# Optimization experiments

Hardware: AMD Instinct MI355X
Metric: run time of the kernel (lower is better)

Reference implementation:

```python
import jax, jax.numpy as jnp
import numpy as np

IN_CH, OUT_CH, MODES1, MODES2 = 64, 64, 32, 32
B, H, W = 16, 256, 256


def setup_inputs() -> dict:
    key = jax.random.key(0)
    k = jax.random.split(key, 5)
    scale = (1.0 / (2 * IN_CH)) ** 0.5
    wshape = (IN_CH, OUT_CH, MODES1, MODES2)
    return {
        "x": jax.random.normal(k[0], (B, IN_CH, H, W), dtype=jnp.float32),
        "weights_pos_re": scale * jax.random.normal(k[1], wshape, dtype=jnp.float32),
        "weights_pos_im": scale * jax.random.normal(k[2], wshape, dtype=jnp.float32),
        "weights_neg_re": scale * jax.random.normal(k[3], wshape, dtype=jnp.float32),
        "weights_neg_im": scale * jax.random.normal(k[4], wshape, dtype=jnp.float32),
        "out_h": H,
        "out_w": W,
    }


def reference(x, weights_pos_re, weights_pos_im, weights_neg_re, weights_neg_im, out_h, out_w):
    b, c_in, in_h, in_w = x.shape
    wp = weights_pos_re + 1j * weights_pos_im  # complex64 [i, o, m1, m2]
    wn = weights_neg_re + 1j * weights_neg_im
    # rfft2 with norm='forward' divides by n (matches torch.fft.rfft2 norm='forward')
    x_ft = jnp.fft.rfft2(x, norm="forward")  # [b, i, in_h, in_w//2+1] complex64
    m1 = min(MODES1, in_h // 2, out_h // 2)
    m2 = min(MODES2, x_ft.shape[-1], out_w // 2 + 1)
    # truncated-mode complex channel mixing on low-frequency corners
    top = jnp.einsum("bixy,ioxy->boxy", x_ft[:, :, :m1, :m2], wp[:, :, :m1, :m2])
    bot = jnp.einsum("bixy,ioxy->boxy", x_ft[:, :, -m1:, :m2], wn[:, :, :m1, :m2])
    out_ft = jnp.zeros((b, OUT_CH, out_h, out_w // 2 + 1), dtype=jnp.complex64)
    out_ft = out_ft.at[:, :, :m1, :m2].set(top)
    out_ft = out_ft.at[:, :, -m1:, :m2].set(bot)
    # irfft2 with norm='forward' multiplies by n
    return jnp.fft.irfft2(out_ft, s=(out_h, out_w), norm="forward")
```

## Files before the change

kernel.cpp:

```cpp
#include <hip/hip_runtime.h>
#include <math.h>

#define PI_F 3.14159265358979323846f


static constexpr int T_FA  = 0;
static constexpr int T_FE  = 16384;
static constexpr int T_FBC = 32768;
static constexpr int T_FBS = 49152;
static constexpr int T_FD1 = 65536;
static constexpr int T_FD2 = 98304;
static constexpr int T_X2  = 131072;
static constexpr int T_CC  = 131072 + 4194304;

typedef __attribute__((ext_vector_type(8))) __bf16 bf16x8;
typedef __attribute__((ext_vector_type(4))) float f32x4;

union B4 { __bf16 b[4]; uint2 u; };

__global__ __launch_bounds__(256) void k_prep(float* __restrict__ ws) {
  int idx = blockIdx.x * 256 + threadIdx.x;
  const float C = 2.0f * PI_F / 256.0f;
  if (idx < 16384) {
    int j = idx;
    int e = j & 7, l = (j >> 3) & 63, q = j >> 9;
    int ns = q & 3, kc = q >> 2;
    int w = kc * 32 + ((l >> 4) & 3) * 8 + e;
    int col = ns * 16 + (l & 15);
    int kxi = col & 31;
    float ang = C * (float)((kxi * w) & 255);
    float v = (col < 32) ? cosf(ang) : -sinf(ang);
    __bf16 hv = (__bf16)v;
    __bf16 lv = (__bf16)(v - (float)hv);
    __bf16* fr = (__bf16*)(ws + T_FA);
    fr[j] = hv; fr[16384 + j] = lv;
  } else if (idx < 32768) {
    int j = idx - 16384;
    int e = j & 7, l = (j >> 3) & 63, q = j >> 9;
    int wb = q & 15, kc = q >> 4;
    int c = kc * 32 + ((l >> 4) & 3) * 8 + e;
    int w = wb * 16 + (l & 15);
    int kxi = (c < 32) ? c : (c - 32);
    float ang = C * (float)((kxi * w) & 255);
    float v = (c < 32) ? cosf(ang) : sinf(ang);
    __bf16 hv = (__bf16)v;
    __bf16 lv = (__bf16)(v - (float)hv);
    __bf16* fr = (__bf16*)(ws + T_FE);
    fr[j] = hv; fr[16384 + j] = lv;
  } else if (idx < 65536) {
    int base = (idx < 49152) ? 32768 : 49152;
    int j = idx - base;
    int e = j & 7, l = (j >> 3) & 63, q = j >> 9;
    int ms4 = q & 3, kc = q >> 2;
    int m = ms4 * 16 + (l & 15);
    int h = kc * 32 + ((l >> 4) & 3) * 8 + e;
    int ky = (m < 32) ? m : (m + 192);
    float ang = C * (float)((ky * h) & 255);
    float v = (idx < 49152) ? cosf(ang) : sinf(ang);
    __bf16 hv = (__bf16)v;
    __bf16 lv = (__bf16)(v - (float)hv);
    __bf16* fr = (__bf16*)(ws + base);
    fr[j] = hv; fr[16384 + j] = lv;
  } else if (idx < 131072) {
    int base = (idx < 98304) ? T_FD1 : T_FD2;
    int j = idx - base;
    int e = j & 7, l = (j >> 3) & 63, f = j >> 9;
    int nsH = f & 3, kc = (f >> 2) & 3, wv = f >> 4;
    int h = wv * 64 + nsH * 16 + (l & 15);
    int k = kc * 32 + ((l >> 4) & 3) * 8 + e;
    int m = (k < 64) ? k : (k - 64);
    int ky = (m < 32) ? m : (m + 192);
    float ang = C * (float)((ky * h) & 255);
    float cv = cosf(ang), sv = sinf(ang);
    float v;
    if (idx < 98304) v = (k < 64) ? cv : -sv;
    else             v = (k < 64) ? -sv : -cv;
    __bf16 hv = (__bf16)v;
    __bf16 lv = (__bf16)(v - (float)hv);
    __bf16* fr = (__bf16*)(ws + base);
    fr[j] = hv; fr[32768 + j] = lv;
  }
}

__device__ __forceinline__ void cvt_split8(const float* __restrict__ p,
                                           bf16x8& h, bf16x8& l) {
  float4 a = *(const float4*)p;
  float4 b = *(const float4*)(p + 4);
#define CVS(e, vv) { __bf16 hh = (__bf16)(vv); h[e] = hh; l[e] = (__bf16)((vv) - (float)hh); }
  CVS(0, a.x) CVS(1, a.y) CVS(2, a.z) CVS(3, a.w)
  CVS(4, b.x) CVS(5, b.y) CVS(6, b.z) CVS(7, b.w)
#undef CVS
}

__global__ __launch_bounds__(256, 2) void k_AB(const float* __restrict__ x,
                                               const float* __restrict__ ws,
                                               float2* __restrict__ X2) {
  __shared__ __bf16 AsH[16384];
  __shared__ __bf16 AsL[16384];
  const __bf16* frA = (const __bf16*)(ws + T_FA);
  const __bf16* fbc = (const __bf16*)(ws + T_FBC);
  const __bf16* fbs = (const __bf16*)(ws + T_FBS);
  const int t = threadIdx.x, bi = blockIdx.x;
  const int l = t & 63, wv = t >> 6;
  const int lr = l & 15, lk = l >> 4;

  f32x4 acc[4][4];
#pragma unroll
  for (int m = 0; m < 4; ++m)
#pragma unroll
    for (int n = 0; n < 4; ++n) acc[m][n] = (f32x4){0.f, 0.f, 0.f, 0.f};
  const float* xb = x + (size_t)bi * 65536 + (size_t)(wv * 64 + lr) * 256 + lk * 8;
  for (int kc = 0; kc < 8; ++kc) {
    bf16x8 ah[4], al[4];
#pragma unroll
    for (int ms = 0; ms < 4; ++ms)
      cvt_split8(xb + ms * 16 * 256 + kc * 32, ah[ms], al[ms]);
    bf16x8 bh[4], bl[4];
#pragma unroll
    for (int ns = 0; ns < 4; ++ns) {
      int fo = ((kc * 4 + ns) * 64 + l) * 8;
      bh[ns] = *(const bf16x8*)(frA + fo);
      bl[ns] = *(const bf16x8*)(frA + 16384 + fo);
    }
#pragma unroll
    for (int ms = 0; ms < 4; ++ms)
#pragma unroll
      for (int ns = 0; ns < 4; ++ns) {
        acc[ms][ns] = __builtin_amdgcn_mfma_f32_16x16x32_bf16(ah[ms], bh[ns], acc[ms][ns], 0, 0, 0);
        acc[ms][ns] = __builtin_amdgcn_mfma_f32_16x16x32_bf16(al[ms], bh[ns], acc[ms][ns], 0, 0, 0);
        acc[ms][ns] = __builtin_amdgcn_mfma_f32_16x16x32_bf16(ah[ms], bl[ns], acc[ms][ns], 0, 0, 0);
      }
  }
#pragma unroll
  for (int ms = 0; ms < 4; ++ms)
#pragma unroll
    for (int ns = 0; ns < 4; ++ns) {
      int kcB = wv * 2 + (ms >> 1);
      int quad = (ms & 1) * 2 + (lk >> 1);
      int base = ((kcB * 4 + ns) * 64 + quad * 16 + lr) * 8 + (lk & 1) * 4;
      B4 ph, pl;
#pragma unroll
      for (int r = 0; r < 4; ++r) {
        float v = acc[ms][ns][r];
        __bf16 hv = (__bf16)v;
        ph.b[r] = hv; pl.b[r] = (__bf16)(v - (float)hv);
      }
      *(uint2*)&AsH[base] = ph.u;
      *(uint2*)&AsL[base] = pl.u;
    }
  __syncthreads();

  f32x4 cyA[4], syA[4];
#pragma unroll
  for (int n = 0; n < 4; ++n) { cyA[n] = (f32x4){0.f,0.f,0.f,0.f}; syA[n] = (f32x4){0.f,0.f,0.f,0.f}; }
  for (int kc = 0; kc < 8; ++kc) {
    bf16x8 Bh[4], Bl[4];
#pragma unroll
    for (int ns = 0; ns < 4; ++ns) {
      int fo = ((kc * 4 + ns) * 64 + l) * 8;
      Bh[ns] = *(const bf16x8*)(AsH + fo);
      Bl[ns] = *(const bf16x8*)(AsL + fo);
    }
    int ao = ((kc * 4 + wv) * 64 + l) * 8;
    bf16x8 cyh = *(const bf16x8*)(fbc + ao);
    bf16x8 cyl = *(const bf16x8*)(fbc + 16384 + ao);
    bf16x8 syh = *(const bf16x8*)(fbs + ao);
    bf16x8 syl = *(const bf16x8*)(fbs + 16384 + ao);
#pragma unroll
    for (int ns = 0; ns < 4; ++ns) {
      cyA[ns] = __builtin_amdgcn_mfma_f32_16x16x32_bf16(cyh, Bh[ns], cyA[ns], 0, 0, 0);
      cyA[ns] = __builtin_amdgcn_mfma_f32_16x16x32_bf16(cyl, Bh[ns], cyA[ns], 0, 0, 0);
      cyA[ns] = __builtin_amdgcn_mfma_f32_16x16x32_bf16(cyh, Bl[ns], cyA[ns], 0, 0, 0);
      syA[ns] = __builtin_amdgcn_mfma_f32_16x16x32_bf16(syh, Bh[ns], syA[ns], 0, 0, 0);
      syA[ns] = __builtin_amdgcn_mfma_f32_16x16x32_bf16(syl, Bh[ns], syA[ns], 0, 0, 0);
      syA[ns] = __builtin_amdgcn_mfma_f32_16x16x32_bf16(syh, Bl[ns], syA[ns], 0, 0, 0);
    }
  }
#pragma unroll
  for (int ns = 0; ns < 2; ++ns)
#pragma unroll
    for (int r = 0; r < 4; ++r) {
      int m = wv * 16 + lk * 4 + r;
      int kx = ns * 16 + lr;
      float re = cyA[ns][r] + syA[ns + 2][r];
      float im = cyA[ns + 2][r] - syA[ns][r];
      X2[(size_t)bi * 2048 + m * 32 + kx] = make_float2(re, im);
    }
}

__global__ __launch_bounds__(256, 4) void k_C(const float2* __restrict__ X2,
                                              const float* __restrict__ wpr,
                                              const float* __restrict__ wpi,
                                              const float* __restrict__ wnr,
                                              const float* __restrict__ wni,
                                              float2* __restrict__ Cc) {
  __shared__ float2 Xs[2][16][32];
  __shared__ float2 Ws[2][4][4][32];
  const int t = threadIdx.x;
  const int mc = blockIdx.x & 63, ot = blockIdx.x >> 6;
  const int mode0 = mc * 32;
  const float *wr, *wi; int wm0;
  if (mode0 < 1024) { wr = wpr; wi = wpi; wm0 = mode0; }
  else              { wr = wnr; wi = wni; wm0 = mode0 - 1024; }
  const int md = t & 31, og2 = (t >> 5) & 1, bq = t >> 6;
  const int bS = t >> 4, c2 = (t & 15) * 2;
  const int e0 = t * 2;
  const int wiS = e0 >> 7, wog = (e0 >> 5) & 3, wmd = e0 & 31;

  float ar[4][2], ai[4][2];
#pragma unroll
  for (int b = 0; b < 4; ++b) { ar[b][0]=0.f; ar[b][1]=0.f; ai[b][0]=0.f; ai[b][1]=0.f; }

  *(float4*)&Xs[0][bS][c2] =
      *(const float4*)&X2[((size_t)(bS * 64 + 0)) * 2048 + mode0 + c2];
  {
    size_t wa = ((size_t)(wiS * 64) + ot * 4 + wog) * 1024 + wm0 + wmd;
    float2 r2 = *(const float2*)&wr[wa];
    float2 i2 = *(const float2*)&wi[wa];
    Ws[0][wiS][wog][wmd]     = make_float2(r2.x, i2.x);
    Ws[0][wiS][wog][wmd + 1] = make_float2(r2.y, i2.y);
  }
  __syncthreads();

  for (int i = 0; i < 64; ++i) {
    const int cur = i & 1, wcur = (i >> 2) & 1;
    if (i < 63)
      *(float4*)&Xs[cur ^ 1][bS][c2] =
          *(const float4*)&X2[((size_t)(bS * 64 + i + 1)) * 2048 + mode0 + c2];
    if ((i & 3) == 0 && i < 60) {
      size_t wa = ((size_t)((i + 4 + wiS) * 64) + ot * 4 + wog) * 1024 + wm0 + wmd;
      float2 r2 = *(const float2*)&wr[wa];
      float2 i2 = *(const float2*)&wi[wa];
      Ws[wcur ^ 1][wiS][wog][wmd]     = make_float2(r2.x, i2.x);
      Ws[wcur ^ 1][wiS][wog][wmd + 1] = make_float2(r2.y, i2.y);
    }
    float2 w0 = Ws[wcur][i & 3][og2 * 2 + 0][md];
    float2 w1 = Ws[wcur][i & 3][og2 * 2 + 1][md];
#pragma unroll
    for (int b = 0; b < 4; ++b) {
      float2 xv = Xs[cur][bq * 4 + b][md];
      ar[b][0] = fmaf(xv.x, w0.x, fmaf(-xv.y, w0.y, ar[b][0]));
      ai[b][0] = fmaf(xv.x, w0.y, fmaf( xv.y, w0.x, ai[b][0]));
      ar[b][1] = fmaf(xv.x, w1.x, fmaf(-xv.y, w1.y, ar[b][1]));
      ai[b][1] = fmaf(xv.x, w1.y, fmaf( xv.y, w1.x, ai[b][1]));
    }
    __syncthreads();
  }

  const float scale = ((md == 0) ? 1.f : 2.f) * (1.f / 65536.f);
#pragma unroll
  for (int b = 0; b < 4; ++b)
#pragma unroll
    for (int o2 = 0; o2 < 2; ++o2)
      Cc[((size_t)((bq * 4 + b) * 64 + ot * 4 + og2 * 2 + o2)) * 2048 + mode0 + md] =
          make_float2(ar[b][o2] * scale, ai[b][o2] * scale);
}

__global__ __launch_bounds__(256, 2) void k_DE(const float2* __restrict__ Cc,
                                               const float* __restrict__ ws,
                                               float* __restrict__ out) {
  __shared__ __bf16 CH[4096], CL[4096];
  __shared__ __bf16 EH[16384], EL[16384];
  const __bf16* fd1 = (const __bf16*)(ws + T_FD1);
  const __bf16* fd2 = (const __bf16*)(ws + T_FD2);
  const __bf16* frE = (const __bf16*)(ws + T_FE);
  const int t = threadIdx.x, bo = blockIdx.x;
  const int l = t & 63, wv = t >> 6;
  const int lr = l & 15, lk = l >> 4;

  const float2* Cp = Cc + (size_t)bo * 2048;
#pragma unroll
  for (int jj = 0; jj < 8; ++jj) {
    int j = t + 256 * jj;
    float2 v = Cp[j];
    int m = j >> 5, kx = j & 31;
    int msK = kx >> 4, lA = ((m >> 3) & 3) * 16 + (kx & 15);
    int e = m & 7, kcR = m >> 5;
    int idxR = ((msK * 4 + kcR) * 64 + lA) * 8 + e;
    int idxI = ((msK * 4 + kcR + 2) * 64 + lA) * 8 + e;
    __bf16 h1 = (__bf16)v.x; CH[idxR] = h1; CL[idxR] = (__bf16)(v.x - (float)h1);
    __bf16 h2 = (__bf16)v.y; CH[idxI] = h2; CL[idxI] = (__bf16)(v.y - (float)h2);
  }
  __syncthreads();

  f32x4 z1[2][4], z2[2][4];
#pragma unroll
  for (int m = 0; m < 2; ++m)
#pragma unroll
    for (int n = 0; n < 4; ++n) { z1[m][n] = (f32x4){0.f,0.f,0.f,0.f}; z2[m][n] = (f32x4){0.f,0.f,0.f,0.f}; }
  for (int kc = 0; kc < 4; ++kc) {
    bf16x8 ah[2], al[2];
#pragma unroll
    for (int msK = 0; msK < 2; ++msK) {
      int fo = ((msK * 4 + kc) * 64 + l) * 8;
      ah[msK] = *(const bf16x8*)(CH + fo);
      al[msK] = *(const bf16x8*)(CL + fo);
    }
#pragma unroll
    for (int nsH = 0; nsH < 4; ++nsH) {
      int bo_ = (((wv * 4 + kc) * 4 + nsH) * 64 + l) * 8;
      bf16x8 b1h = *(const bf16x8*)(fd1 + bo_);
      bf16x8 b1l = *(const bf16x8*)(fd1 + 32768 + bo_);
      bf16x8 b2h = *(const bf16x8*)(fd2 + bo_);
      bf16x8 b2l = *(const bf16x8*)(fd2 + 32768 + bo_);
#pragma unroll
      for (int msK = 0; msK < 2; ++msK) {
        z1[msK][nsH] = __builtin_amdgcn_mfma_f32_16x16x32_bf16(ah[msK], b1h, z1[msK][nsH], 0, 0, 0);
        z1[msK][nsH] = __builtin_amdgcn_mfma_f32_16x16x32_bf16(al[msK], b1h, z1[msK][nsH], 0, 0, 0);
        z1[msK][nsH] = __builtin_amdgcn_mfma_f32_16x16x32_bf16(ah[msK], b1l, z1[msK][nsH], 0, 0, 0);
        z2[msK][nsH] = __builtin_amdgcn_mfma_f32_16x16x32_bf16(ah[msK], b2h, z2[msK][nsH], 0, 0, 0);
        z2[msK][nsH] = __builtin_amdgcn_mfma_f32_16x16x32_bf16(al[msK], b2h, z2[msK][nsH], 0, 0, 0);
        z2[msK][nsH] = __builtin_amdgcn_mfma_f32_16x16x32_bf16(ah[msK], b2l, z2[msK][nsH], 0, 0, 0);
      }
    }
  }
#pragma unroll
  for (int msK = 0; msK < 2; ++msK)
#pragma unroll
    for (int nsH = 0; nsH < 4; ++nsH) {
      int lp = (msK * 2 + (lk >> 1)) * 16 + lr;
      int eb = (lk & 1) * 4;
      int base1 = (((wv * 4 + nsH) * 2 + 0) * 64 + lp) * 8 + eb;
      int base2 = (((wv * 4 + nsH) * 2 + 1) * 64 + lp) * 8 + eb;
      B4 p1h, p1l, p2h, p2l;
#pragma unroll
      for (int r = 0; r < 4; ++r) {
        float v1 = z1[msK][nsH][r];
        __bf16 h1 = (__bf16)v1; p1h.b[r] = h1; p1l.b[r] = (__bf16)(v1 - (float)h1);
        float v2 = z2[msK][nsH][r];
        __bf16 h2 = (__bf16)v2; p2h.b[r] = h2; p2l.b[r] = (__bf16)(v2 - (float)h2);
      }
      *(uint2*)&EH[base1] = p1h.u; *(uint2*)&EL[base1] = p1l.u;
      *(uint2*)&EH[base2] = p2h.u; *(uint2*)&EL[base2] = p2l.u;
    }
  __syncthreads();

  bf16x8 ah[4][2], al[4][2];
#pragma unroll
  for (int ms = 0; ms < 4; ++ms)
#pragma unroll
    for (int kc = 0; kc < 2; ++kc) {
      int fo = (((wv * 4 + ms) * 2 + kc) * 64 + l) * 8;
      ah[ms][kc] = *(const bf16x8*)(EH + fo);
      al[ms][kc] = *(const bf16x8*)(EL + fo);
    }
  float* ob = out + (size_t)bo * 65536;
  for (int cb = 0; cb < 4; ++cb) {
    f32x4 eacc[4][4];
#pragma unroll
    for (int m = 0; m < 4; ++m)
#pragma unroll
      for (int n = 0; n < 4; ++n) eacc[m][n] = (f32x4){0.f, 0.f, 0.f, 0.f};
#pragma unroll
    for (int kc = 0; kc < 2; ++kc) {
      bf16x8 bh[4], bl[4];
#pragma unroll
      for (int ns = 0; ns < 4; ++ns) {
        int fo = ((kc * 16 + cb * 4 + ns) * 64 + l) * 8;
        bh[ns] = *(const bf16x8*)(frE + fo);
        bl[ns] = *(const bf16x8*)(frE + 16384 + fo);
      }
#pragma unroll
      for (int ms = 0; ms < 4; ++ms)
#pragma unroll
        for (int ns = 0; ns < 4; ++ns) {
          eacc[ms][ns] = __builtin_amdgcn_mfma_f32_16x16x32_bf16(ah[ms][kc], bh[ns], eacc[ms][ns], 0, 0, 0);
          eacc[ms][ns] = __builtin_amdgcn_mfma_f32_16x16x32_bf16(al[ms][kc], bh[ns], eacc[ms][ns], 0, 0, 0);
          eacc[ms][ns] = __builtin_amdgcn_mfma_f32_16x16x32_bf16(ah[ms][kc], bl[ns], eacc[ms][ns], 0, 0, 0);
        }
    }
#pragma unroll
    for (int ms = 0; ms < 4; ++ms)
#pragma unroll
      for (int ns = 0; ns < 4; ++ns) {
        int col = cb * 64 + ns * 16 + lr;
        int row0 = wv * 64 + ms * 16 + lk * 4;
#pragma unroll
        for (int r = 0; r < 4; ++r)
          ob[(size_t)(row0 + r) * 256 + col] = eacc[ms][ns][r];
      }
  }
}

extern "C" void kernel_launch(void* const* d_in, const int* in_sizes, int n_in,
                              void* d_out, int out_size, void* d_ws, size_t ws_size,
                              hipStream_t stream) {
  (void)in_sizes; (void)n_in; (void)out_size; (void)ws_size;
  const float* x   = (const float*)d_in[0];
  const float* wpr = (const float*)d_in[1];
  const float* wpi = (const float*)d_in[2];
  const float* wnr = (const float*)d_in[3];
  const float* wni = (const float*)d_in[4];
  float* out = (float*)d_out;
  float* ws  = (float*)d_ws;

  float2* X2 = (float2*)(ws + T_X2);
  float2* Cc = (float2*)(ws + T_CC);

  k_prep<<<512, 256, 0, stream>>>(ws);
  k_AB<<<1024, 256, 0, stream>>>(x, ws, X2);
  k_C<<<1024, 256, 0, stream>>>(X2, wpr, wpi, wnr, wni, Cc);
  k_DE<<<1024, 256, 0, stream>>>(Cc, ws, out);
}
```

Baseline: 219.5 us.

## Halve LDS staging in k_AB and k_DE to raise occupancy to three blocks

k_AB now processes the row DFT in two halves of 128 rows. Each half's intermediate is staged into a half-sized LDS buffer and immediately consumed by the column DFT, with accumulators carried across halves. k_DE aliases its C and E buffers in one shared array and writes and consumes the E intermediate in two passes, which halves per-block LDS and register tiles. Both kernels raise launch bounds to three blocks per CU to improve latency hiding, at the cost of extra syncthreads, more passes and tighter register budgets.

```diff
diff --git a/kernel.cpp b/kernel.cpp
--- a/kernel.cpp
+++ b/kernel.cpp
@@ -92,11 +92,11 @@
 #undef CVS
 }
 
-__global__ __launch_bounds__(256, 2) void k_AB(const float* __restrict__ x,
+__global__ __launch_bounds__(256, 3) void k_AB(const float* __restrict__ x,
                                                const float* __restrict__ ws,
                                                float2* __restrict__ X2) {
-  __shared__ __bf16 AsH[16384];
-  __shared__ __bf16 AsL[16384];
+  __shared__ __bf16 AsH[8192];
+  __shared__ __bf16 AsL[8192];
   const __bf16* frA = (const __bf16*)(ws + T_FA);
   const __bf16* fbc = (const __bf16*)(ws + T_FBC);
   const __bf16* fbs = (const __bf16*)(ws + T_FBS);
@@ -104,76 +104,78 @@
   const int l = t & 63, wv = t >> 6;
   const int lr = l & 15, lk = l >> 4;
 
-  f32x4 acc[4][4];
-#pragma unroll
-  for (int m = 0; m < 4; ++m)
-#pragma unroll
-    for (int n = 0; n < 4; ++n) acc[m][n] = (f32x4){0.f, 0.f, 0.f, 0.f};
-  const float* xb = x + (size_t)bi * 65536 + (size_t)(wv * 64 + lr) * 256 + lk * 8;
-  for (int kc = 0; kc < 8; ++kc) {
-    bf16x8 ah[4], al[4];
-#pragma unroll
-    for (int ms = 0; ms < 4; ++ms)
-      cvt_split8(xb + ms * 16 * 256 + kc * 32, ah[ms], al[ms]);
-    bf16x8 bh[4], bl[4];
-#pragma unroll
-    for (int ns = 0; ns < 4; ++ns) {
-      int fo = ((kc * 4 + ns) * 64 + l) * 8;
-      bh[ns] = *(const bf16x8*)(frA + fo);
-      bl[ns] = *(const bf16x8*)(frA + 16384 + fo);
-    }
-#pragma unroll
-    for (int ms = 0; ms < 4; ++ms)
+  f32x4 cyA[4], syA[4];
+#pragma unroll
+  for (int n = 0; n < 4; ++n) { cyA[n] = (f32x4){0.f,0.f,0.f,0.f}; syA[n] = (f32x4){0.f,0.f,0.f,0.f}; }
+
+  for (int hh = 0; hh < 2; ++hh) {
+    f32x4 acc[2][4];
+#pragma unroll
+    for (int m = 0; m < 2; ++m)
+#pragma unroll
+      for (int n = 0; n < 4; ++n) acc[m][n] = (f32x4){0.f, 0.f, 0.f, 0.f};
+    const float* xb = x + (size_t)bi * 65536 + (size_t)(hh * 128 + wv * 32 + lr) * 256 + lk * 8;
+    for (int kc = 0; kc < 8; ++kc) {
+      bf16x8 ah[2], al[2];
+#pragma unroll
+      for (int ms = 0; ms < 2; ++ms)
+        cvt_split8(xb + ms * 16 * 256 + kc * 32, ah[ms], al[ms]);
+      bf16x8 bh[4], bl[4];
 #pragma unroll
       for (int ns = 0; ns < 4; ++ns) {
-        acc[ms][ns] = __builtin_amdgcn_mfma_f32_16x16x32_bf16(ah[ms], bh[ns], acc[ms][ns], 0, 0, 0);
-        acc[ms][ns] = __builtin_amdgcn_mfma_f32_16x16x32_bf16(al[ms], bh[ns], acc[ms][ns], 0, 0, 0);
-        acc[ms][ns] = __builtin_amdgcn_mfma_f32_16x16x32_bf16(ah[ms], bl[ns], acc[ms][ns], 0, 0, 0);
-      }
-  }
-#pragma unroll
-  for (int ms = 0; ms < 4; ++ms)
-#pragma unroll
-    for (int ns = 0; ns < 4; ++ns) {
-      int kcB = wv * 2 + (ms >> 1);
-      int quad = (ms & 1) * 2 + (lk >> 1);
-      int base = ((kcB * 4 + ns) * 64 + quad * 16 + lr) * 8 + (lk & 1) * 4;
-      B4 ph, pl;
-#pragma unroll
-      for (int r = 0; r < 4; ++r) {
-        float v = acc[ms][ns][r];
-        __bf16 hv = (__bf16)v;
-        ph.b[r] = hv; pl.b[r] = (__bf16)(v - (float)hv);
-      }
-      *(uint2*)&AsH[base] = ph.u;
-      *(uint2*)&AsL[base] = pl.u;
-    }
-  __syncthreads();
-
-  f32x4 cyA[4], syA[4];
-#pragma unroll
-  for (int n = 0; n < 4; ++n) { cyA[n] = (f32x4){0.f,0.f,0.f,0.f}; syA[n] = (f32x4){0.f,0.f,0.f,0.f}; }
-  for (int kc = 0; kc < 8; ++kc) {
-    bf16x8 Bh[4], Bl[4];
-#pragma unroll
-    for (int ns = 0; ns < 4; ++ns) {
-      int fo = ((kc * 4 + ns) * 64 + l) * 8;
-      Bh[ns] = *(const bf16x8*)(AsH + fo);
-      Bl[ns] = *(const bf16x8*)(AsL + fo);
-    }
-    int ao = ((kc * 4 + wv) * 64 + l) * 8;
-    bf16x8 cyh = *(const bf16x8*)(fbc + ao);
-    bf16x8 cyl = *(const bf16x8*)(fbc + 16384 + ao);
-    bf16x8 syh = *(const bf16x8*)(fbs + ao);
-    bf16x8 syl = *(const bf16x8*)(fbs + 16384 + ao);
-#pragma unroll
-    for (int ns = 0; ns < 4; ++ns) {
-      cyA[ns] = __builtin_amdgcn_mfma_f32_16x16x32_bf16(cyh, Bh[ns], cyA[ns], 0, 0, 0);
-      cyA[ns] = __builtin_amdgcn_mfma_f32_16x16x32_bf16(cyl, Bh[ns], cyA[ns], 0, 0, 0);
-      cyA[ns] = __builtin_amdgcn_mfma_f32_16x16x32_bf16(cyh, Bl[ns], cyA[ns], 0, 0, 0);
-      syA[ns] = __builtin_amdgcn_mfma_f32_16x16x32_bf16(syh, Bh[ns], syA[ns], 0, 0, 0);
-      syA[ns] = __builtin_amdgcn_mfma_f32_16x16x32_bf16(syl, Bh[ns], syA[ns], 0, 0, 0);
-      syA[ns] = __builtin_amdgcn_mfma_f32_16x16x32_bf16(syh, Bl[ns], syA[ns], 0, 0, 0);
+        int fo = ((kc * 4 + ns) * 64 + l) * 8;
+        bh[ns] = *(const bf16x8*)(frA + fo);
+        bl[ns] = *(const bf16x8*)(frA + 16384 + fo);
+      }
+#pragma unroll
+      for (int ms = 0; ms < 2; ++ms)
+#pragma unroll
+        for (int ns = 0; ns < 4; ++ns) {
+          acc[ms][ns] = __builtin_amdgcn_mfma_f32_16x16x32_bf16(ah[ms], bh[ns], acc[ms][ns], 0, 0, 0);
+          acc[ms][ns] = __builtin_amdgcn_mfma_f32_16x16x32_bf16(al[ms], bh[ns], acc[ms][ns], 0, 0, 0);
+          acc[ms][ns] = __builtin_amdgcn_mfma_f32_16x16x32_bf16(ah[ms], bl[ns], acc[ms][ns], 0, 0, 0);
+        }
+    }
+    __syncthreads();
+#pragma unroll
+    for (int ms = 0; ms < 2; ++ms)
+#pragma unroll
+      for (int ns = 0; ns < 4; ++ns) {
+        int lp = (ms * 2 + (lk >> 1)) * 16 + lr;
+        int base = ((wv * 4 + ns) * 64 + lp) * 8 + (lk & 1) * 4;
+        B4 ph, pl;
+#pragma unroll
+        for (int r = 0; r < 4; ++r) {
+          float v = acc[ms][ns][r];
+          __bf16 hv = (__bf16)v;
+          ph.b[r] = hv; pl.b[r] = (__bf16)(v - (float)hv);
+        }
+        *(uint2*)&AsH[base] = ph.u;
+        *(uint2*)&AsL[base] = pl.u;
+      }
+    __syncthreads();
+    for (int kc_l = 0; kc_l < 4; ++kc_l) {
+      bf16x8 Bh[4], Bl[4];
+#pragma unroll
+      for (int ns = 0; ns < 4; ++ns) {
+        int fo = ((kc_l * 4 + ns) * 64 + l) * 8;
+        Bh[ns] = *(const bf16x8*)(AsH + fo);
+        Bl[ns] = *(const bf16x8*)(AsL + fo);
+      }
+      int ao = (((hh * 4 + kc_l) * 4 + wv) * 64 + l) * 8;
+      bf16x8 cyh = *(const bf16x8*)(fbc + ao);
+      bf16x8 cyl = *(const bf16x8*)(fbc + 16384 + ao);
+      bf16x8 syh = *(const bf16x8*)(fbs + ao);
+      bf16x8 syl = *(const bf16x8*)(fbs + 16384 + ao);
+#pragma unroll
+      for (int ns = 0; ns < 4; ++ns) {
+        cyA[ns] = __builtin_amdgcn_mfma_f32_16x16x32_bf16(cyh, Bh[ns], cyA[ns], 0, 0, 0);
+        cyA[ns] = __builtin_amdgcn_mfma_f32_16x16x32_bf16(cyl, Bh[ns], cyA[ns], 0, 0, 0);
+        cyA[ns] = __builtin_amdgcn_mfma_f32_16x16x32_bf16(cyh, Bl[ns], cyA[ns], 0, 0, 0);
+        syA[ns] = __builtin_amdgcn_mfma_f32_16x16x32_bf16(syh, Bh[ns], syA[ns], 0, 0, 0);
+        syA[ns] = __builtin_amdgcn_mfma_f32_16x16x32_bf16(syl, Bh[ns], syA[ns], 0, 0, 0);
+        syA[ns] = __builtin_amdgcn_mfma_f32_16x16x32_bf16(syh, Bl[ns], syA[ns], 0, 0, 0);
+      }
     }
   }
 #pragma unroll
@@ -256,11 +258,14 @@
           make_float2(ar[b][o2] * scale, ai[b][o2] * scale);
 }
 
-__global__ __launch_bounds__(256, 2) void k_DE(const float2* __restrict__ Cc,
+__global__ __launch_bounds__(256, 3) void k_DE(const float2* __restrict__ Cc,
                                                const float* __restrict__ ws,
                                                float* __restrict__ out) {
-  __shared__ __bf16 CH[4096], CL[4096];
-  __shared__ __bf16 EH[16384], EL[16384];
+  __shared__ __bf16 smem[16384];
+  __bf16* CH = smem;
+  __bf16* CL = smem + 4096;
+  __bf16* EH = smem;
+  __bf16* EL = smem + 8192;
   const __bf16* fd1 = (const __bf16*)(ws + T_FD1);
   const __bf16* fd2 = (const __bf16*)(ws + T_FD2);
   const __bf16* frE = (const __bf16*)(ws + T_FE);
@@ -314,71 +319,74 @@
       }
     }
   }
-#pragma unroll
-  for (int msK = 0; msK < 2; ++msK)
-#pragma unroll
-    for (int nsH = 0; nsH < 4; ++nsH) {
-      int lp = (msK * 2 + (lk >> 1)) * 16 + lr;
-      int eb = (lk & 1) * 4;
-      int base1 = (((wv * 4 + nsH) * 2 + 0) * 64 + lp) * 8 + eb;
-      int base2 = (((wv * 4 + nsH) * 2 + 1) * 64 + lp) * 8 + eb;
-      B4 p1h, p1l, p2h, p2l;
-#pragma unroll
-      for (int r = 0; r < 4; ++r) {
-        float v1 = z1[msK][nsH][r];
-        __bf16 h1 = (__bf16)v1; p1h.b[r] = h1; p1l.b[r] = (__bf16)(v1 - (float)h1);
-        float v2 = z2[msK][nsH][r];
-        __bf16 h2 = (__bf16)v2; p2h.b[r] = h2; p2l.b[r] = (__bf16)(v2 - (float)h2);
-      }
-      *(uint2*)&EH[base1] = p1h.u; *(uint2*)&EL[base1] = p1l.u;
-      *(uint2*)&EH[base2] = p2h.u; *(uint2*)&EL[base2] = p2l.u;
-    }
   __syncthreads();
 
-  bf16x8 ah[4][2], al[4][2];
-#pragma unroll
-  for (int ms = 0; ms < 4; ++ms)
-#pragma unroll
-    for (int kc = 0; kc < 2; ++kc) {
-      int fo = (((wv * 4 + ms) * 2 + kc) * 64 + l) * 8;
-      ah[ms][kc] = *(const bf16x8*)(EH + fo);
-      al[ms][kc] = *(const bf16x8*)(EL + fo);
-    }
   float* ob = out + (size_t)bo * 65536;
-  for (int cb = 0; cb < 4; ++cb) {
-    f32x4 eacc[4][4];
-#pragma unroll
-    for (int m = 0; m < 4; ++m)
-#pragma unroll
-      for (int n = 0; n < 4; ++n) eacc[m][n] = (f32x4){0.f, 0.f, 0.f, 0.f};
-#pragma unroll
-    for (int kc = 0; kc < 2; ++kc) {
-      bf16x8 bh[4], bl[4];
-#pragma unroll
-      for (int ns = 0; ns < 4; ++ns) {
-        int fo = ((kc * 16 + cb * 4 + ns) * 64 + l) * 8;
-        bh[ns] = *(const bf16x8*)(frE + fo);
-        bl[ns] = *(const bf16x8*)(frE + 16384 + fo);
-      }
-#pragma unroll
-      for (int ms = 0; ms < 4; ++ms)
+  for (int p = 0; p < 2; ++p) {
+#pragma unroll
+    for (int msK = 0; msK < 2; ++msK)
+#pragma unroll
+      for (int q = 0; q < 2; ++q) {
+        int nsH = 2 * p + q;
+        int lp = (msK * 2 + (lk >> 1)) * 16 + lr;
+        int eb = (lk & 1) * 4;
+        int base1 = (((wv * 2 + q) * 2 + 0) * 64 + lp) * 8 + eb;
+        int base2 = (((wv * 2 + q) * 2 + 1) * 64 + lp) * 8 + eb;
+        B4 p1h, p1l, p2h, p2l;
+#pragma unroll
+        for (int r = 0; r < 4; ++r) {
+          float v1 = z1[msK][nsH][r];
+          __bf16 h1 = (__bf16)v1; p1h.b[r] = h1; p1l.b[r] = (__bf16)(v1 - (float)h1);
+          float v2 = z2[msK][nsH][r];
+          __bf16 h2 = (__bf16)v2; p2h.b[r] = h2; p2l.b[r] = (__bf16)(v2 - (float)h2);
+        }
+        *(uint2*)&EH[base1] = p1h.u; *(uint2*)&EL[base1] = p1l.u;
+        *(uint2*)&EH[base2] = p2h.u; *(uint2*)&EL[base2] = p2l.u;
+      }
+    bf16x8 ah[2][2], al[2][2];
+#pragma unroll
+    for (int q = 0; q < 2; ++q)
+#pragma unroll
+      for (int kc = 0; kc < 2; ++kc) {
+        int fo = (((wv * 2 + q) * 2 + kc) * 64 + l) * 8;
+        ah[q][kc] = *(const bf16x8*)(EH + fo);
+        al[q][kc] = *(const bf16x8*)(EL + fo);
+      }
+    for (int cb = 0; cb < 4; ++cb) {
+      f32x4 eacc[2][4];
+#pragma unroll
+      for (int m = 0; m < 2; ++m)
+#pragma unroll
+        for (int n = 0; n < 4; ++n) eacc[m][n] = (f32x4){0.f, 0.f, 0.f, 0.f};
+#pragma unroll
+      for (int kc = 0; kc < 2; ++kc) {
+        bf16x8 bh[4], bl[4];
 #pragma unroll
         for (int ns = 0; ns < 4; ++ns) {
-          eacc[ms][ns] = __builtin_amdgcn_mfma_f32_16x16x32_bf16(ah[ms][kc], bh[ns], eacc[ms][ns], 0, 0, 0);
-          eacc[ms][ns] = __builtin_amdgcn_mfma_f32_16x16x32_bf16(al[ms][kc], bh[ns], eacc[ms][ns], 0, 0, 0);
-          eacc[ms][ns] = __builtin_amdgcn_mfma_f32_16x16x32_bf16(ah[ms][kc], bl[ns], eacc[ms][ns], 0, 0, 0);
+          int fo = ((kc * 16 + cb * 4 + ns) * 64 + l) * 8;
+          bh[ns] = *(const bf16x8*)(frE + fo);
+          bl[ns] = *(const bf16x8*)(frE + 16384 + fo);
         }
-    }
-#pragma unroll
-    for (int ms = 0; ms < 4; ++ms)
-#pragma unroll
-      for (int ns = 0; ns < 4; ++ns) {
-        int col = cb * 64 + ns * 16 + lr;
-        int row0 = wv * 64 + ms * 16 + lk * 4;
-#pragma unroll
-        for (int r = 0; r < 4; ++r)
-          ob[(size_t)(row0 + r) * 256 + col] = eacc[ms][ns][r];
-      }
+#pragma unroll
+        for (int q = 0; q < 2; ++q)
+#pragma unroll
+          for (int ns = 0; ns < 4; ++ns) {
+            eacc[q][ns] = __builtin_amdgcn_mfma_f32_16x16x32_bf16(ah[q][kc], bh[ns], eacc[q][ns], 0, 0, 0);
+            eacc[q][ns] = __builtin_amdgcn_mfma_f32_16x16x32_bf16(al[q][kc], bh[ns], eacc[q][ns], 0, 0, 0);
+            eacc[q][ns] = __builtin_amdgcn_mfma_f32_16x16x32_bf16(ah[q][kc], bl[ns], eacc[q][ns], 0, 0, 0);
+          }
+      }
+#pragma unroll
+      for (int q = 0; q < 2; ++q)
+#pragma unroll
+        for (int ns = 0; ns < 4; ++ns) {
+          int col = cb * 64 + ns * 16 + lr;
+          int row0 = wv * 64 + (2 * p + q) * 16 + lk * 4;
+#pragma unroll
+          for (int r = 0; r < 4; ++r)
+            ob[(size_t)(row0 + r) * 256 + col] = eacc[q][ns][r];
+        }
+    }
   }
 }
 
```

Result: slower. 373.1 us (+70.0%).
